# Performance work log

Hardware: AMD Instinct MI355X
Metric: run time of the kernel (lower is better)

## Reference

```python
import jax, jax.numpy as jnp
import numpy as np

THRESHOLD = 2.0
PRED_STEPS = 30
MODE_NUM = 6
B, N = 128, 4096


def setup_inputs() -> dict:
    key = jax.random.key(0)
    k1, k2, k3 = jax.random.split(key, 3)
    goals_scores = jax.random.normal(k1, (B, N), dtype=jnp.float32)
    # scale goals so typical spacing is comparable to the 2.0 m NMS threshold
    pred_goals = jax.random.normal(k2, (B, 2, N), dtype=jnp.float32) * 20.0
    traj_preds = jax.random.normal(k3, (B, PRED_STEPS * 2, N), dtype=jnp.float32)
    return {"goals_scores": goals_scores, "traj_preds": traj_preds, "pred_goals": pred_goals}


def _select_one(scores, trajs, goals):
    # scores: [N], trajs: [2*P, N], goals: [2, N]
    order = jnp.argsort(-scores)                       # descending sort by score
    s = scores[order]                                  # [N]
    g = goals.T[order]                                 # [N, 2]
    t = trajs.T[order].reshape(-1, PRED_STEPS, 2)      # [N, P, 2]
    n = g.shape[0]
    thresh2 = jnp.float32(THRESHOLD * THRESHOLD)

    def step(carry, inp):
        sel_goals, sel_idx, count = carry
        gi, i = inp
        # squared distance to already-selected goals (inf-init => never suppressed when empty)
        d2 = jnp.sum((sel_goals - gi) ** 2, axis=-1)   # [MODE_NUM]
        suppressed = jnp.min(d2) < thresh2             # strict <, matches original
        take = jnp.logical_and(jnp.logical_not(suppressed), count < MODE_NUM)
        slot = jnp.logical_and(jnp.arange(MODE_NUM) == count, take)
        sel_goals = jnp.where(slot[:, None], gi, sel_goals)
        sel_idx = jnp.where(slot, i, sel_idx)
        count = count + take.astype(count.dtype)
        return (sel_goals, sel_idx, count), None

    init = (
        jnp.full((MODE_NUM, 2), 1e9, dtype=g.dtype),
        jnp.zeros((MODE_NUM,), dtype=jnp.int32),
        jnp.int32(0),
    )
    (sel_goals, sel_idx, count), _ = jax.lax.scan(
        step, init, (g, jnp.arange(n, dtype=jnp.int32))
    )
    # unfilled slots fall back to the top-scored candidate (index 0 in sorted order)
    sel_idx = jnp.where(jnp.arange(MODE_NUM) < count, sel_idx, 0)
    return t[sel_idx], s[sel_idx]                      # [MODE_NUM, P, 2], [MODE_NUM]


def reference(goals_scores, traj_preds, pred_goals):
    # returns (pred_trajs [B, MODE_NUM, P, 2], scores [B, MODE_NUM])
    return jax.vmap(_select_one)(goals_scores, traj_preds, pred_goals)
```

## Files before the change

kernel.cpp:

```cpp
#include <hip/hip_runtime.h>
#include <stdint.h>


namespace {
constexpr int kB        = 128;
constexpr int kN        = 4096;
constexpr int kSteps    = 30;
constexpr int kModes    = 6;
constexpr int kTPB      = 256;
constexpr int kPerThread = kN / kTPB;
constexpr float kThresh2 = 4.0f;
}

__device__ __forceinline__ unsigned int order_key(float f) {
    unsigned int u = __float_as_uint(f);
    return (u & 0x80000000u) ? ~u : (u | 0x80000000u);
}

__device__ __forceinline__ unsigned long long shfl_down_u64(unsigned long long v, int off) {
    unsigned int lo = (unsigned int)(v & 0xFFFFFFFFull);
    unsigned int hi = (unsigned int)(v >> 32);
    lo = __shfl_down(lo, off, 64);
    hi = __shfl_down(hi, off, 64);
    return (((unsigned long long)hi) << 32) | (unsigned long long)lo;
}

__global__ __launch_bounds__(kTPB)
void densetnt_nms_kernel(const float* __restrict__ scores,
                         const float* __restrict__ trajs,
                         const float* __restrict__ goals,
                         float* __restrict__ out) {
    const int b    = blockIdx.x;
    const int tid  = threadIdx.x;
    const int lane = tid & 63;

    __shared__ unsigned long long s_maxkey[kModes];
    __shared__ int   s_selidx[kModes];
    __shared__ float s_selscore[kModes];
    __shared__ int   s_count;

    const float* sc = scores + (size_t)b * kN;
    const float* gx = goals  + (size_t)b * 2 * kN;
    const float* gy = gx + kN;

    float my_sc[kPerThread], my_gx[kPerThread], my_gy[kPerThread];
    #pragma unroll
    for (int j = 0; j < kPerThread; ++j) {
        int i = tid + j * kTPB;
        my_sc[j] = sc[i];
        my_gx[j] = gx[i];
        my_gy[j] = gy[i];
    }

    if (tid < kModes) s_maxkey[tid] = 0ULL;
    if (tid == 0) s_count = 0;
    __syncthreads();

    unsigned int valid = 0xFFFFu;

    for (int m = 0; m < kModes; ++m) {
        unsigned long long best = 0ULL;
        #pragma unroll
        for (int j = 0; j < kPerThread; ++j) {
            if (valid & (1u << j)) {
                int i = tid + j * kTPB;
                unsigned long long key =
                    (((unsigned long long)order_key(my_sc[j])) << 32) |
                    (unsigned long long)(0xFFFFFFFFu - (unsigned int)i);
                best = key > best ? key : best;
            }
        }
        #pragma unroll
        for (int off = 32; off > 0; off >>= 1) {
            unsigned long long o = shfl_down_u64(best, off);
            best = o > best ? o : best;
        }
        if (lane == 0 && best != 0ULL) atomicMax(&s_maxkey[m], best);
        __syncthreads();

        unsigned long long k = s_maxkey[m];
        if (k != 0ULL) {
            int idx = (int)(0xFFFFFFFFu - (unsigned int)(k & 0xFFFFFFFFull));
            if (tid == 0) {
                s_selidx[m]   = idx;
                s_selscore[m] = sc[idx];
                s_count       = m + 1;
            }
            float sxv = gx[idx];
            float syv = gy[idx];
            #pragma unroll
            for (int j = 0; j < kPerThread; ++j) {
                if (valid & (1u << j)) {
                    float dx = my_gx[j] - sxv;
                    float dy = my_gy[j] - syv;
                    if (dx * dx + dy * dy < kThresh2) valid &= ~(1u << j);
                }
            }
        }
    }
    __syncthreads();

    if (tid == 0) {
        for (int m = s_count; m < kModes; ++m) {
            s_selidx[m]   = s_selidx[0];
            s_selscore[m] = s_selscore[0];
        }
    }
    __syncthreads();

    const float* tb   = trajs + (size_t)b * (2 * kSteps) * kN;
    float*       outt = out   + (size_t)b * kModes * (2 * kSteps);
    for (int e = tid; e < kModes * 2 * kSteps; e += kTPB) {
        int m  = e / (2 * kSteps);
        int pc = e - m * (2 * kSteps);
        outt[e] = tb[(size_t)pc * kN + s_selidx[m]];
    }
    if (tid < kModes) {
        out[(size_t)kB * kModes * 2 * kSteps + (size_t)b * kModes + tid] = s_selscore[tid];
    }
}

extern "C" void kernel_launch(void* const* d_in, const int* in_sizes, int n_in,
                              void* d_out, int out_size, void* d_ws, size_t ws_size,
                              hipStream_t stream) {
    const float* scores = (const float*)d_in[0];
    const float* trajs  = (const float*)d_in[1];
    const float* goals  = (const float*)d_in[2];
    float* out = (float*)d_out;
    densetnt_nms_kernel<<<kB, kTPB, 0, stream>>>(scores, trajs, goals, out);
}
```

Baseline: 167.9 us.

## Use 1024-thread blocks with float4 loads and broadcast winner goal via LDS

Each block now runs 1024 threads, each owning four contiguous candidates loaded with float4 vector loads instead of sixteen strided scalars. The owner thread of each selected candidate writes its goal coordinates and score to shared memory, so the global re-reads of the winner are gone, at the cost of one extra barrier per mode. The aim is to cut per-thread serial work and latency in this single-wave-per-batch, latency-bound kernel. The trade-off is that the block-level reduction now spans more wavefronts and more atomics per mode.

```diff
diff --git a/kernel.cpp b/kernel.cpp
--- a/kernel.cpp
+++ b/kernel.cpp
@@ -3,12 +3,12 @@
 
 
 namespace {
-constexpr int kB        = 128;
-constexpr int kN        = 4096;
-constexpr int kSteps    = 30;
-constexpr int kModes    = 6;
-constexpr int kTPB      = 256;
-constexpr int kPerThread = kN / kTPB;
+constexpr int kB      = 128;
+constexpr int kN      = 4096;
+constexpr int kSteps  = 30;
+constexpr int kModes  = 6;
+constexpr int kTPB    = 1024;
+constexpr int kPer    = kN / kTPB;
 constexpr float kThresh2 = 4.0f;
 }
 
@@ -37,36 +37,35 @@
     __shared__ unsigned long long s_maxkey[kModes];
     __shared__ int   s_selidx[kModes];
     __shared__ float s_selscore[kModes];
+    __shared__ float s_gx, s_gy;
     __shared__ int   s_count;
 
-    const float* sc = scores + (size_t)b * kN;
-    const float* gx = goals  + (size_t)b * 2 * kN;
-    const float* gy = gx + kN;
+    const float4* sc4 = (const float4*)(scores + (size_t)b * kN);
+    const float4* gx4 = (const float4*)(goals  + (size_t)b * 2 * kN);
+    const float4* gy4 = (const float4*)(goals  + (size_t)b * 2 * kN + kN);
 
-    float my_sc[kPerThread], my_gx[kPerThread], my_gy[kPerThread];
-    #pragma unroll
-    for (int j = 0; j < kPerThread; ++j) {
-        int i = tid + j * kTPB;
-        my_sc[j] = sc[i];
-        my_gx[j] = gx[i];
-        my_gy[j] = gy[i];
-    }
+    float4 vsc = sc4[tid];
+    float4 vgx = gx4[tid];
+    float4 vgy = gy4[tid];
+    float my_sc[kPer] = {vsc.x, vsc.y, vsc.z, vsc.w};
+    float my_gx[kPer] = {vgx.x, vgx.y, vgx.z, vgx.w};
+    float my_gy[kPer] = {vgy.x, vgy.y, vgy.z, vgy.w};
 
     if (tid < kModes) s_maxkey[tid] = 0ULL;
     if (tid == 0) s_count = 0;
     __syncthreads();
 
-    unsigned int valid = 0xFFFFu;
+    unsigned int valid = 0xFu;
 
     for (int m = 0; m < kModes; ++m) {
         unsigned long long best = 0ULL;
         #pragma unroll
-        for (int j = 0; j < kPerThread; ++j) {
-            if (valid & (1u << j)) {
-                int i = tid + j * kTPB;
+        for (int c = 0; c < kPer; ++c) {
+            if (valid & (1u << c)) {
+                unsigned int i = (unsigned int)(tid * kPer + c);
                 unsigned long long key =
-                    (((unsigned long long)order_key(my_sc[j])) << 32) |
-                    (unsigned long long)(0xFFFFFFFFu - (unsigned int)i);
+                    (((unsigned long long)order_key(my_sc[c])) << 32) |
+                    (unsigned long long)(0xFFFFFFFFu - i);
                 best = key > best ? key : best;
             }
         }
@@ -78,27 +77,33 @@
         if (lane == 0 && best != 0ULL) atomicMax(&s_maxkey[m], best);
         __syncthreads();
 
-        unsigned long long k = s_maxkey[m];
+        const unsigned long long k = s_maxkey[m];
+        int idx = -1;
         if (k != 0ULL) {
-            int idx = (int)(0xFFFFFFFFu - (unsigned int)(k & 0xFFFFFFFFull));
-            if (tid == 0) {
+            idx = (int)(0xFFFFFFFFu - (unsigned int)(k & 0xFFFFFFFFull));
+            if (tid == (idx >> 2)) {
+                const int c = idx & 3;
+                s_gx = my_gx[c];
+                s_gy = my_gy[c];
                 s_selidx[m]   = idx;
-                s_selscore[m] = sc[idx];
+                s_selscore[m] = my_sc[c];
                 s_count       = m + 1;
             }
-            float sxv = gx[idx];
-            float syv = gy[idx];
+        }
+        __syncthreads();
+
+        if (k != 0ULL) {
+            const float sxv = s_gx, syv = s_gy;
             #pragma unroll
-            for (int j = 0; j < kPerThread; ++j) {
-                if (valid & (1u << j)) {
-                    float dx = my_gx[j] - sxv;
-                    float dy = my_gy[j] - syv;
-                    if (dx * dx + dy * dy < kThresh2) valid &= ~(1u << j);
+            for (int c = 0; c < kPer; ++c) {
+                if (valid & (1u << c)) {
+                    float dx = my_gx[c] - sxv;
+                    float dy = my_gy[c] - syv;
+                    if (dx * dx + dy * dy < kThresh2) valid &= ~(1u << c);
                 }
             }
         }
     }
-    __syncthreads();
 
     if (tid == 0) {
         for (int m = s_count; m < kModes; ++m) {
@@ -110,10 +115,10 @@
 
     const float* tb   = trajs + (size_t)b * (2 * kSteps) * kN;
     float*       outt = out   + (size_t)b * kModes * (2 * kSteps);
-    for (int e = tid; e < kModes * 2 * kSteps; e += kTPB) {
-        int m  = e / (2 * kSteps);
-        int pc = e - m * (2 * kSteps);
-        outt[e] = tb[(size_t)pc * kN + s_selidx[m]];
+    if (tid < kModes * 2 * kSteps) {
+        int m  = tid / (2 * kSteps);
+        int pc = tid - m * (2 * kSteps);
+        outt[tid] = tb[(size_t)pc * kN + s_selidx[m]];
     }
     if (tid < kModes) {
         out[(size_t)kB * kModes * 2 * kSteps + (size_t)b * kModes + tid] = s_selscore[tid];
```

New measurement: 166.5 us. No clear change (-0.8%).
